# Optimization experiments

Measured on AMD Instinct MI355X. Metric: run time of the kernel, lower is better.

## Reference

```python
import jax, jax.numpy as jnp
import numpy as np

N_SAMPLES = 128
AGENTS = 64
D = 128          # latent_size
EDIM = 2         # edge attr dim
N = N_SAMPLES * AGENTS
EPS = 1e-5


def _build_edges():
    a = np.arange(AGENTS)
    rows = np.repeat(a, AGENTS)
    cols = np.tile(a, AGENTS)
    mask = rows != cols  # fully connected, no self loops
    rows, cols = rows[mask], cols[mask]
    offsets = (np.arange(N_SAMPLES) * AGENTS)[:, None]
    src = (rows[None, :] + offsets).ravel().astype(np.int32)  # edge_index[0]
    dst = (cols[None, :] + offsets).ravel().astype(np.int32)  # edge_index[1]
    return src, dst


def setup_inputs() -> dict:
    key = jax.random.key(0)
    ks = jax.random.split(key, 16)
    src, dst = _build_edges()
    zin = 2 * D + EDIM  # CGConv concat [x_i, x_j, e]
    inp = {
        "gnn_in": jax.random.normal(ks[0], (N, D), jnp.float32),
        "centers": jax.random.normal(ks[1], (N, EDIM), jnp.float32),
        "edge_src": jnp.asarray(src),
        "edge_dst": jnp.asarray(dst),
    }
    for li, base in ((1, 2), (2, 8)):
        inp[f"Wf{li}"] = jax.random.normal(ks[base + 0], (zin, D), jnp.float32) / np.sqrt(zin)
        inp[f"bf{li}"] = jnp.zeros((D,), jnp.float32)
        inp[f"Ws{li}"] = jax.random.normal(ks[base + 1], (zin, D), jnp.float32) / np.sqrt(zin)
        inp[f"bs{li}"] = jnp.zeros((D,), jnp.float32)
        inp[f"gamma{li}"] = jnp.ones((D,), jnp.float32)
        inp[f"beta{li}"] = jnp.zeros((D,), jnp.float32)
    return inp


def _cgconv(x, e, src, dst, Wf, bf, Ws, bs, gamma, beta):
    # message: z = [x_i(target), x_j(source), e]; sigmoid(Wf z) * softplus(Ws z)
    z = jnp.concatenate([x[dst], x[src], e], axis=-1)  # [E, 2D+2]
    m = jax.nn.sigmoid(z @ Wf + bf) * jax.nn.softplus(z @ Ws + bs)
    agg = jax.ops.segment_sum(m, dst, num_segments=N)  # scatter-add at targets
    # batch norm (training-mode batch stats) then residual, as in PyG CGConv
    mu = agg.mean(axis=0)
    var = agg.var(axis=0)
    agg = (agg - mu) * jax.lax.rsqrt(var + EPS) * gamma + beta
    return agg + x


def reference(gnn_in, centers, edge_src, edge_dst,
              Wf1, bf1, Ws1, bs1, gamma1, beta1,
              Wf2, bf2, Ws2, bs2, gamma2, beta2):
    # edge_attr = centers[col] - centers[row]
    e = centers[edge_dst] - centers[edge_src]  # [E, 2]
    x = jax.nn.relu(_cgconv(gnn_in, e, edge_src, edge_dst, Wf1, bf1, Ws1, bs1, gamma1, beta1))
    x = jax.nn.relu(_cgconv(x, e, edge_src, edge_dst, Wf2, bf2, Ws2, bs2, gamma2, beta2))
    return x
```

## Files before the change

kernel.cpp:

```cpp
#include <hip/hip_runtime.h>
#include <hip/hip_bf16.h>

#define NSAMP 128
#define AGENTS 64
#define D 128
#define NN (NSAMP * AGENTS)
#define LOG2E 1.44269504088896340736f
#define LN2   0.69314718055994530942f
#define EPSF  1e-5f

typedef __attribute__((ext_vector_type(8))) short short8;
typedef __attribute__((ext_vector_type(4))) float floatx4;

__device__ __forceinline__ float bf2f(unsigned short u) {
    unsigned v = ((unsigned)u) << 16;
    float f; __builtin_memcpy(&f, &v, 4); return f;
}
__device__ __forceinline__ unsigned short f2bf(float f) {
    unsigned x; __builtin_memcpy(&x, &f, 4);
    return (unsigned short)((x + 0x7FFFu + ((x >> 16) & 1u)) >> 16);
}

__global__ __launch_bounds__(256) void cvt_kernel(
    const float* __restrict__ x0,
    const float* __restrict__ Wf1, const float* __restrict__ Ws1,
    const float* __restrict__ Wf2, const float* __restrict__ Ws2,
    unsigned short* __restrict__ Xb, unsigned short* __restrict__ WT)
{
    int b = blockIdx.x;
    if (b < 512) {
        int off = (b * 256 + threadIdx.x) * 8;
        float4 v0 = *(const float4*)&x0[off];
        float4 v1 = *(const float4*)&x0[off + 4];
        short8 s;
        s[0] = (short)f2bf(v0.x); s[1] = (short)f2bf(v0.y);
        s[2] = (short)f2bf(v0.z); s[3] = (short)f2bf(v0.w);
        s[4] = (short)f2bf(v1.x); s[5] = (short)f2bf(v1.y);
        s[6] = (short)f2bf(v1.z); s[7] = (short)f2bf(v1.w);
        *(short8*)&Xb[off] = s;
    } else {
        int wb = b - 512;
        int rr = wb * 16 + (threadIdx.x >> 4);
        int kk = (threadIdx.x & 15) * 8;
        int layer = rr >> 9, rem = rr & 511, arr = rem >> 7, c = rem & 127;
        const float* M = (arr < 2) ? (layer ? Wf2 : Wf1) : (layer ? Ws2 : Ws1);
        int side = arr & 1;
        short8 s;
        #pragma unroll
        for (int j = 0; j < 8; ++j)
            s[j] = (short)f2bf(M[(size_t)(side * 128 + kk + j) * D + c]);
        *(short8*)&WT[(size_t)(layer * 4 + arr) * 16384 + c * 128 + kk] = s;
    }
}

__global__ __launch_bounds__(256) void prep_mfma(
    const unsigned short* __restrict__ Xb,
    const unsigned short* __restrict__ WT,
    const float* __restrict__ centers,
    const float* __restrict__ Wf, const float* __restrict__ bf_,
    const float* __restrict__ Ws, const float* __restrict__ bs_,
    unsigned short* __restrict__ out)
{
    const int m0   = blockIdx.x * 16;
    const int wv   = threadIdx.x >> 6;
    const int lane = threadIdx.x & 63;
    const int quad = lane >> 4, l16 = lane & 15;

    short8 a[4];
    const unsigned short* xrow = Xb + (size_t)(m0 + l16) * 128 + quad * 8;
    #pragma unroll
    for (int kc = 0; kc < 4; ++kc) a[kc] = *(const short8*)(xrow + kc * 32);

    float ce0[4], ce1[4];
    #pragma unroll
    for (int r = 0; r < 4; ++r) {
        int n = m0 + quad * 4 + r;
        ce0[r] = centers[2 * n]; ce1[r] = centers[2 * n + 1];
    }

    const float sgn   = (wv & 1) ? -1.f : 1.f;
    const float scale = (wv < 2) ? -LOG2E : LOG2E;
    const float* Wsrc = (wv < 2) ? Wf : Ws;
    const float* bias = (wv == 0) ? bf_ : ((wv == 2) ? bs_ : nullptr);
    const unsigned short* Wa = WT + (size_t)wv * 16384;
    unsigned short* ob = out + (size_t)wv * NN * 128;

    for (int nt = 0; nt < 8; ++nt) {
        const int n0 = nt * 16;
        short8 bfr[4];
        const unsigned short* wrow = Wa + (size_t)(n0 + l16) * 128 + quad * 8;
        #pragma unroll
        for (int kc = 0; kc < 4; ++kc) bfr[kc] = *(const short8*)(wrow + kc * 32);

        floatx4 acc = {0.f, 0.f, 0.f, 0.f};
        #pragma unroll
        for (int kc = 0; kc < 4; ++kc)
            acc = __builtin_amdgcn_mfma_f32_16x16x32_bf16(a[kc], bfr[kc], acc, 0, 0, 0);

        const int col = n0 + l16;
        const float cw0 = Wsrc[256 * D + col];
        const float cw1 = Wsrc[257 * D + col];
        const float bv  = bias ? bias[col] : 0.f;
        #pragma unroll
        for (int r = 0; r < 4; ++r) {
            float t = acc[r] + bv + sgn * fmaf(ce0[r], cw0, ce1[r] * cw1);
            ob[(size_t)(m0 + quad * 4 + r) * 128 + col] =
                f2bf(__builtin_amdgcn_exp2f(scale * t));
        }
    }
}

__global__ __launch_bounds__(256) void edge_kernel(
    const unsigned short* __restrict__ EAf, const unsigned short* __restrict__ EBf,
    const unsigned short* __restrict__ EAs, const unsigned short* __restrict__ EBs,
    float* __restrict__ agg,
    float* __restrict__ partials)
{
    const int s = blockIdx.x >> 2;
    const int g = blockIdx.x & 3;
    const int tid = threadIdx.x;
    const int c  = tid & 127;
    const int dh = tid >> 7;
    const int nbase = s * AGENTS;

    __shared__ float Bfs[AGENTS][D];
    __shared__ float Bss[AGENTS][D];

    #pragma unroll
    for (int i = 0; i < 4; ++i) {
        int f8 = i * 256 + tid;
        int idx = f8 * 8;
        int j = idx >> 7, cc = idx & 127;
        short8 vf = *(const short8*)&EBf[(size_t)(nbase + j) * D + cc];
        short8 vs = *(const short8*)&EBs[(size_t)(nbase + j) * D + cc];
        float4 f0, f1, s0, s1v;
        f0.x = bf2f((unsigned short)vf[0]); f0.y = bf2f((unsigned short)vf[1]);
        f0.z = bf2f((unsigned short)vf[2]); f0.w = bf2f((unsigned short)vf[3]);
        f1.x = bf2f((unsigned short)vf[4]); f1.y = bf2f((unsigned short)vf[5]);
        f1.z = bf2f((unsigned short)vf[6]); f1.w = bf2f((unsigned short)vf[7]);
        s0.x = bf2f((unsigned short)vs[0]); s0.y = bf2f((unsigned short)vs[1]);
        s0.z = bf2f((unsigned short)vs[2]); s0.w = bf2f((unsigned short)vs[3]);
        s1v.x = bf2f((unsigned short)vs[4]); s1v.y = bf2f((unsigned short)vs[5]);
        s1v.z = bf2f((unsigned short)vs[6]); s1v.w = bf2f((unsigned short)vs[7]);
        *(float4*)&Bfs[j][cc]     = f0;
        *(float4*)&Bfs[j][cc + 4] = f1;
        *(float4*)&Bss[j][cc]     = s0;
        *(float4*)&Bss[j][cc + 4] = s1v;
    }
    __syncthreads();

    const int d0 = g * 16 + dh * 8;
    float eaf[8], eas[8], acc[8];
    #pragma unroll
    for (int i = 0; i < 8; ++i) {
        int n = nbase + d0 + i;
        eaf[i] = bf2f(EAf[(size_t)n * D + c]);
        eas[i] = bf2f(EAs[(size_t)n * D + c]);
        acc[i] = 0.f;
    }

    for (int j = 0; j < AGENTS; ++j) {
        float ebf = Bfs[j][c];
        float ebs = Bss[j][c];
        #pragma unroll
        for (int i = 0; i < 8; ++i) {
            float sg = __builtin_amdgcn_rcpf(1.f + eaf[i] * ebf);
            float lg = __builtin_amdgcn_logf(1.f + eas[i] * ebs);
            acc[i] += sg * lg;
        }
    }

    float s1 = 0.f, s2 = 0.f;
    #pragma unroll
    for (int i = 0; i < 8; ++i) {
        int j = d0 + i;
        float sg = __builtin_amdgcn_rcpf(1.f + eaf[i] * Bfs[j][c]);
        float lg = __builtin_amdgcn_logf(1.f + eas[i] * Bss[j][c]);
        float a = (acc[i] - sg * lg) * LN2;
        agg[(size_t)(nbase + d0 + i) * D + c] = a;
        s1 += a;
        s2 += a * a;
    }

    __syncthreads();
    if (dh == 1) { Bfs[0][c] = s1; Bss[0][c] = s2; }
    __syncthreads();
    if (dh == 0) {
        s1 += Bfs[0][c];
        s2 += Bss[0][c];
        partials[(size_t)blockIdx.x * 256 + c]       = s1;
        partials[(size_t)blockIdx.x * 256 + 128 + c] = s2;
    }
}

__global__ __launch_bounds__(256) void stats_kernel(
    const float* __restrict__ partials, float* __restrict__ stats)
{
    const int c = blockIdx.x;
    const int t = threadIdx.x;
    float s1 = partials[(size_t)t * 256 + c] + partials[(size_t)(t + 256) * 256 + c];
    float s2 = partials[(size_t)t * 256 + 128 + c] + partials[(size_t)(t + 256) * 256 + 128 + c];
    __shared__ float r1[256], r2[256];
    r1[t] = s1; r2[t] = s2;
    __syncthreads();
    for (int off = 128; off > 0; off >>= 1) {
        if (t < off) { r1[t] += r1[t + off]; r2[t] += r2[t + off]; }
        __syncthreads();
    }
    if (t == 0) {
        float mu = r1[0] * (1.f / NN);
        float var = r2[0] * (1.f / NN) - mu * mu;
        stats[c]     = mu;
        stats[D + c] = rsqrtf(var + EPSF);
    }
}

__global__ __launch_bounds__(256) void bncvt_kernel(
    const float* __restrict__ agg, const float* __restrict__ xin,
    const float* __restrict__ stats,
    const float* __restrict__ gamma, const float* __restrict__ beta,
    float* __restrict__ x1, unsigned short* __restrict__ Xb)
{
    const int t = blockIdx.x * 256 + threadIdx.x;
    const int n = t >> 4;
    const int c = (t & 15) * 8;
    size_t off = (size_t)n * D + c;
    float v[8]; short8 s;
    #pragma unroll
    for (int h = 0; h < 2; ++h) {
        float4 a  = *(const float4*)&agg[off + h * 4];
        float4 xv = *(const float4*)&xin[off + h * 4];
        float4 mu = *(const float4*)&stats[c + h * 4];
        float4 rs = *(const float4*)&stats[D + c + h * 4];
        float4 gm = *(const float4*)&gamma[c + h * 4];
        float4 bt = *(const float4*)&beta[c + h * 4];
        v[h*4+0] = fmaxf(0.f, fmaf((a.x - mu.x) * rs.x, gm.x, bt.x) + xv.x);
        v[h*4+1] = fmaxf(0.f, fmaf((a.y - mu.y) * rs.y, gm.y, bt.y) + xv.y);
        v[h*4+2] = fmaxf(0.f, fmaf((a.z - mu.z) * rs.z, gm.z, bt.z) + xv.z);
        v[h*4+3] = fmaxf(0.f, fmaf((a.w - mu.w) * rs.w, gm.w, bt.w) + xv.w);
    }
    *(float4*)&x1[off]     = *(float4*)&v[0];
    *(float4*)&x1[off + 4] = *(float4*)&v[4];
    #pragma unroll
    for (int e = 0; e < 8; ++e) s[e] = (short)f2bf(v[e]);
    *(short8*)&Xb[off] = s;
}

__global__ __launch_bounds__(256) void bn_kernel(
    const float* __restrict__ agg, const float* __restrict__ xin,
    const float* __restrict__ stats,
    const float* __restrict__ gamma, const float* __restrict__ beta,
    float* __restrict__ outp)
{
    const int t = blockIdx.x * 256 + threadIdx.x;
    const int n = t >> 5;
    const int c = (t & 31) * 4;
    float4 a  = *(const float4*)&agg[(size_t)n * D + c];
    float4 xv = *(const float4*)&xin[(size_t)n * D + c];
    float4 mu = *(const float4*)&stats[c];
    float4 rs = *(const float4*)&stats[D + c];
    float4 gm = *(const float4*)&gamma[c];
    float4 bt = *(const float4*)&beta[c];
    float4 o;
    o.x = fmaxf(0.f, fmaf((a.x - mu.x) * rs.x, gm.x, bt.x) + xv.x);
    o.y = fmaxf(0.f, fmaf((a.y - mu.y) * rs.y, gm.y, bt.y) + xv.y);
    o.z = fmaxf(0.f, fmaf((a.z - mu.z) * rs.z, gm.z, bt.z) + xv.z);
    o.w = fmaxf(0.f, fmaf((a.w - mu.w) * rs.w, gm.w, bt.w) + xv.w);
    *(float4*)&outp[(size_t)n * D + c] = o;
}

extern "C" void kernel_launch(void* const* d_in, const int* in_sizes, int n_in,
                              void* d_out, int out_size, void* d_ws, size_t ws_size,
                              hipStream_t stream) {
    const float* x0      = (const float*)d_in[0];
    const float* centers = (const float*)d_in[1];
    const float* Wf[2] = { (const float*)d_in[4],  (const float*)d_in[10] };
    const float* bf[2] = { (const float*)d_in[5],  (const float*)d_in[11] };
    const float* Ws[2] = { (const float*)d_in[6],  (const float*)d_in[12] };
    const float* bs[2] = { (const float*)d_in[7],  (const float*)d_in[13] };
    const float* gm[2] = { (const float*)d_in[8],  (const float*)d_in[14] };
    const float* bt[2] = { (const float*)d_in[9],  (const float*)d_in[15] };

    const size_t ND = (size_t)NN * D;
    unsigned short* ws_u = (unsigned short*)d_ws;
    unsigned short* Xb = ws_u;
    unsigned short* WT = ws_u + ND;
    unsigned short* AB = WT + 2 * 65536;
    float* fbase    = (float*)(AB + 4 * ND);
    float* agg      = fbase;
    float* x1       = fbase + ND;
    float* partials = fbase + 2 * ND;
    float* stats    = partials + 512 * 256;

    float* outp = (float*)d_out;

    cvt_kernel<<<dim3(576), dim3(256), 0, stream>>>(
        x0, Wf[0], Ws[0], Wf[1], Ws[1], Xb, WT);

    prep_mfma<<<dim3(512), dim3(256), 0, stream>>>(
        Xb, WT, centers, Wf[0], bf[0], Ws[0], bs[0], AB);
    edge_kernel<<<dim3(512), dim3(256), 0, stream>>>(
        AB, AB + ND, AB + 2 * ND, AB + 3 * ND, agg, partials);
    stats_kernel<<<dim3(128), dim3(256), 0, stream>>>(partials, stats);
    bncvt_kernel<<<dim3(512), dim3(256), 0, stream>>>(
        agg, x0, stats, gm[0], bt[0], x1, Xb);

    prep_mfma<<<dim3(512), dim3(256), 0, stream>>>(
        Xb, WT + 65536, centers, Wf[1], bf[1], Ws[1], bs[1], AB);
    edge_kernel<<<dim3(512), dim3(256), 0, stream>>>(
        AB, AB + ND, AB + 2 * ND, AB + 3 * ND, agg, partials);
    stats_kernel<<<dim3(128), dim3(256), 0, stream>>>(partials, stats);
    bn_kernel<<<dim3(1024), dim3(256), 0, stream>>>(
        agg, x1, stats, gm[1], bt[1], outp);
}
```

Measured before the change: 165.2 us.

## Fuse projection GEMM into edge kernel and replace stats pass with atomics

Merges the MFMA projection kernel into the edge kernel. Each block now computes its sample's source-side exponentials directly into shared memory as packed bf16 pairs, and computes the target-side values for its own 16 rows, so the bf16 intermediate buffers never go through global memory. The separate stats reduction kernel is replaced by per-block atomicAdd into a zeroed accumulator, with mean and rsqrt folded into the BN kernels. This saves two launches per layer and the intermediate traffic. In exchange, each of the 4 blocks per sample recomputes the 64-row source GEMM, and float atomics make the sums order-nondeterministic.

```diff
diff --git a/kernel.cpp b/kernel.cpp
--- a/kernel.cpp
+++ b/kernel.cpp
@@ -12,8 +12,7 @@
 typedef __attribute__((ext_vector_type(8))) short short8;
 typedef __attribute__((ext_vector_type(4))) float floatx4;
 
-__device__ __forceinline__ float bf2f(unsigned short u) {
-    unsigned v = ((unsigned)u) << 16;
+__device__ __forceinline__ float u2f(unsigned v) {
     float f; __builtin_memcpy(&f, &v, 4); return f;
 }
 __device__ __forceinline__ unsigned short f2bf(float f) {
@@ -25,7 +24,8 @@
     const float* __restrict__ x0,
     const float* __restrict__ Wf1, const float* __restrict__ Ws1,
     const float* __restrict__ Wf2, const float* __restrict__ Ws2,
-    unsigned short* __restrict__ Xb, unsigned short* __restrict__ WT)
+    unsigned short* __restrict__ Xb, unsigned short* __restrict__ WT,
+    float* __restrict__ sacc)
 {
     int b = blockIdx.x;
     if (b < 512) {
@@ -38,7 +38,7 @@
         s[4] = (short)f2bf(v1.x); s[5] = (short)f2bf(v1.y);
         s[6] = (short)f2bf(v1.z); s[7] = (short)f2bf(v1.w);
         *(short8*)&Xb[off] = s;
-    } else {
+    } else if (b < 576) {
         int wb = b - 512;
         int rr = wb * 16 + (threadIdx.x >> 4);
         int kk = (threadIdx.x & 15) * 8;
@@ -50,174 +50,147 @@
         for (int j = 0; j < 8; ++j)
             s[j] = (short)f2bf(M[(size_t)(side * 128 + kk + j) * D + c]);
         *(short8*)&WT[(size_t)(layer * 4 + arr) * 16384 + c * 128 + kk] = s;
-    }
-}
-
-__global__ __launch_bounds__(256) void prep_mfma(
+    } else {
+        sacc[threadIdx.x]       = 0.f;
+        sacc[256 + threadIdx.x] = 0.f;
+    }
+}
+
+__global__ __launch_bounds__(256) void prep_edge(
     const unsigned short* __restrict__ Xb,
     const unsigned short* __restrict__ WT,
     const float* __restrict__ centers,
     const float* __restrict__ Wf, const float* __restrict__ bf_,
     const float* __restrict__ Ws, const float* __restrict__ bs_,
-    unsigned short* __restrict__ out)
-{
-    const int m0   = blockIdx.x * 16;
-    const int wv   = threadIdx.x >> 6;
-    const int lane = threadIdx.x & 63;
+    float* __restrict__ agg,
+    float* __restrict__ sacc)
+{
+    const int s = blockIdx.x >> 2, g = blockIdx.x & 3;
+    const int nbase = s * AGENTS;
+    const int tid = threadIdx.x, wv = tid >> 6, lane = tid & 63;
     const int quad = lane >> 4, l16 = lane & 15;
 
-    short8 a[4];
-    const unsigned short* xrow = Xb + (size_t)(m0 + l16) * 128 + quad * 8;
-    #pragma unroll
-    for (int kc = 0; kc < 4; ++kc) a[kc] = *(const short8*)(xrow + kc * 32);
-
-    float ce0[4], ce1[4];
-    #pragma unroll
-    for (int r = 0; r < 4; ++r) {
-        int n = m0 + quad * 4 + r;
-        ce0[r] = centers[2 * n]; ce1[r] = centers[2 * n + 1];
-    }
-
-    const float sgn   = (wv & 1) ? -1.f : 1.f;
-    const float scale = (wv < 2) ? -LOG2E : LOG2E;
-    const float* Wsrc = (wv < 2) ? Wf : Ws;
-    const float* bias = (wv == 0) ? bf_ : ((wv == 2) ? bs_ : nullptr);
-    const unsigned short* Wa = WT + (size_t)wv * 16384;
-    unsigned short* ob = out + (size_t)wv * NN * 128;
-
-    for (int nt = 0; nt < 8; ++nt) {
-        const int n0 = nt * 16;
-        short8 bfr[4];
-        const unsigned short* wrow = Wa + (size_t)(n0 + l16) * 128 + quad * 8;
-        #pragma unroll
-        for (int kc = 0; kc < 4; ++kc) bfr[kc] = *(const short8*)(wrow + kc * 32);
-
-        floatx4 acc = {0.f, 0.f, 0.f, 0.f};
-        #pragma unroll
-        for (int kc = 0; kc < 4; ++kc)
-            acc = __builtin_amdgcn_mfma_f32_16x16x32_bf16(a[kc], bfr[kc], acc, 0, 0, 0);
-
-        const int col = n0 + l16;
-        const float cw0 = Wsrc[256 * D + col];
-        const float cw1 = Wsrc[257 * D + col];
-        const float bv  = bias ? bias[col] : 0.f;
+    __shared__ float        EAls[2][16][132];
+    __shared__ unsigned int EBpk[64][132];
+
+    short8 wBf[2][4], wBs[2][4];
+    float cwf0[2], cwf1[2], cws0[2], cws1[2], bfv[2], bsv[2];
+    #pragma unroll
+    for (int p = 0; p < 2; ++p) {
+        const int col = wv * 32 + p * 16 + l16;
+        const unsigned short* w1 = WT + (size_t)1 * 16384 + (size_t)col * 128 + quad * 8;
+        const unsigned short* w3 = WT + (size_t)3 * 16384 + (size_t)col * 128 + quad * 8;
+        #pragma unroll
+        for (int kc = 0; kc < 4; ++kc) {
+            wBf[p][kc] = *(const short8*)(w1 + kc * 32);
+            wBs[p][kc] = *(const short8*)(w3 + kc * 32);
+        }
+        cwf0[p] = Wf[256 * D + col]; cwf1[p] = Wf[257 * D + col];
+        cws0[p] = Ws[256 * D + col]; cws1[p] = Ws[257 * D + col];
+        bfv[p] = bf_[col]; bsv[p] = bs_[col];
+    }
+
+    for (int m = 0; m < 4; ++m) {
+        short8 a[4];
+        const unsigned short* xr = Xb + (size_t)(nbase + m * 16 + l16) * 128 + quad * 8;
+        #pragma unroll
+        for (int kc = 0; kc < 4; ++kc) a[kc] = *(const short8*)(xr + kc * 32);
+        float ce0[4], ce1[4];
         #pragma unroll
         for (int r = 0; r < 4; ++r) {
-            float t = acc[r] + bv + sgn * fmaf(ce0[r], cw0, ce1[r] * cw1);
-            ob[(size_t)(m0 + quad * 4 + r) * 128 + col] =
-                f2bf(__builtin_amdgcn_exp2f(scale * t));
-        }
-    }
-}
-
-__global__ __launch_bounds__(256) void edge_kernel(
-    const unsigned short* __restrict__ EAf, const unsigned short* __restrict__ EBf,
-    const unsigned short* __restrict__ EAs, const unsigned short* __restrict__ EBs,
-    float* __restrict__ agg,
-    float* __restrict__ partials)
-{
-    const int s = blockIdx.x >> 2;
-    const int g = blockIdx.x & 3;
-    const int tid = threadIdx.x;
-    const int c  = tid & 127;
-    const int dh = tid >> 7;
-    const int nbase = s * AGENTS;
-
-    __shared__ float Bfs[AGENTS][D];
-    __shared__ float Bss[AGENTS][D];
-
-    #pragma unroll
-    for (int i = 0; i < 4; ++i) {
-        int f8 = i * 256 + tid;
-        int idx = f8 * 8;
-        int j = idx >> 7, cc = idx & 127;
-        short8 vf = *(const short8*)&EBf[(size_t)(nbase + j) * D + cc];
-        short8 vs = *(const short8*)&EBs[(size_t)(nbase + j) * D + cc];
-        float4 f0, f1, s0, s1v;
-        f0.x = bf2f((unsigned short)vf[0]); f0.y = bf2f((unsigned short)vf[1]);
-        f0.z = bf2f((unsigned short)vf[2]); f0.w = bf2f((unsigned short)vf[3]);
-        f1.x = bf2f((unsigned short)vf[4]); f1.y = bf2f((unsigned short)vf[5]);
-        f1.z = bf2f((unsigned short)vf[6]); f1.w = bf2f((unsigned short)vf[7]);
-        s0.x = bf2f((unsigned short)vs[0]); s0.y = bf2f((unsigned short)vs[1]);
-        s0.z = bf2f((unsigned short)vs[2]); s0.w = bf2f((unsigned short)vs[3]);
-        s1v.x = bf2f((unsigned short)vs[4]); s1v.y = bf2f((unsigned short)vs[5]);
-        s1v.z = bf2f((unsigned short)vs[6]); s1v.w = bf2f((unsigned short)vs[7]);
-        *(float4*)&Bfs[j][cc]     = f0;
-        *(float4*)&Bfs[j][cc + 4] = f1;
-        *(float4*)&Bss[j][cc]     = s0;
-        *(float4*)&Bss[j][cc + 4] = s1v;
+            int n = nbase + m * 16 + quad * 4 + r;
+            ce0[r] = centers[2 * n]; ce1[r] = centers[2 * n + 1];
+        }
+        #pragma unroll
+        for (int p = 0; p < 2; ++p) {
+            floatx4 aF = {0.f,0.f,0.f,0.f}, aS = {0.f,0.f,0.f,0.f};
+            #pragma unroll
+            for (int kc = 0; kc < 4; ++kc) {
+                aF = __builtin_amdgcn_mfma_f32_16x16x32_bf16(a[kc], wBf[p][kc], aF, 0,0,0);
+                aS = __builtin_amdgcn_mfma_f32_16x16x32_bf16(a[kc], wBs[p][kc], aS, 0,0,0);
+            }
+            const int col = wv * 32 + p * 16 + l16;
+            #pragma unroll
+            for (int r = 0; r < 4; ++r) {
+                float ctf = fmaf(ce0[r], cwf0[p], ce1[r] * cwf1[p]);
+                float cts = fmaf(ce0[r], cws0[p], ce1[r] * cws1[p]);
+                unsigned uf = (unsigned)f2bf(__builtin_amdgcn_exp2f(-LOG2E * (aF[r] - ctf)));
+                unsigned us = (unsigned)f2bf(__builtin_amdgcn_exp2f( LOG2E * (aS[r] - cts)));
+                EBpk[m * 16 + quad * 4 + r][col] = uf | (us << 16);
+            }
+        }
+        if (m == g) {
+            #pragma unroll
+            for (int p = 0; p < 2; ++p) {
+                const int col = wv * 32 + p * 16 + l16;
+                const unsigned short* w0 = WT + (size_t)col * 128 + quad * 8;
+                const unsigned short* w2 = WT + (size_t)2 * 16384 + (size_t)col * 128 + quad * 8;
+                floatx4 aF = {0.f,0.f,0.f,0.f}, aS = {0.f,0.f,0.f,0.f};
+                #pragma unroll
+                for (int kc = 0; kc < 4; ++kc) {
+                    short8 f0 = *(const short8*)(w0 + kc * 32);
+                    short8 f2 = *(const short8*)(w2 + kc * 32);
+                    aF = __builtin_amdgcn_mfma_f32_16x16x32_bf16(a[kc], f0, aF, 0,0,0);
+                    aS = __builtin_amdgcn_mfma_f32_16x16x32_bf16(a[kc], f2, aS, 0,0,0);
+                }
+                #pragma unroll
+                for (int r = 0; r < 4; ++r) {
+                    float ctf = fmaf(ce0[r], cwf0[p], ce1[r] * cwf1[p]);
+                    float cts = fmaf(ce0[r], cws0[p], ce1[r] * cws1[p]);
+                    EAls[0][quad * 4 + r][col] =
+                        __builtin_amdgcn_exp2f(-LOG2E * (aF[r] + ctf + bfv[p]));
+                    EAls[1][quad * 4 + r][col] =
+                        __builtin_amdgcn_exp2f( LOG2E * (aS[r] + cts + bsv[p]));
+                }
+            }
+        }
     }
     __syncthreads();
 
-    const int d0 = g * 16 + dh * 8;
+    const int c = tid & 127, dh = tid >> 7;
     float eaf[8], eas[8], acc[8];
     #pragma unroll
     for (int i = 0; i < 8; ++i) {
-        int n = nbase + d0 + i;
-        eaf[i] = bf2f(EAf[(size_t)n * D + c]);
-        eas[i] = bf2f(EAs[(size_t)n * D + c]);
+        eaf[i] = EAls[0][dh * 8 + i][c];
+        eas[i] = EAls[1][dh * 8 + i][c];
         acc[i] = 0.f;
     }
-
-    for (int j = 0; j < AGENTS; ++j) {
-        float ebf = Bfs[j][c];
-        float ebs = Bss[j][c];
+    for (int j = 0; j < 64; ++j) {
+        unsigned pk = EBpk[j][c];
+        float ebf = u2f(pk << 16);
+        float ebs = u2f(pk & 0xFFFF0000u);
         #pragma unroll
         for (int i = 0; i < 8; ++i) {
-            float sg = __builtin_amdgcn_rcpf(1.f + eaf[i] * ebf);
-            float lg = __builtin_amdgcn_logf(1.f + eas[i] * ebs);
-            acc[i] += sg * lg;
-        }
-    }
-
+            float sg = __builtin_amdgcn_rcpf(fmaf(eaf[i], ebf, 1.f));
+            float lg = __builtin_amdgcn_logf(fmaf(eas[i], ebs, 1.f));
+            acc[i] = fmaf(sg, lg, acc[i]);
+        }
+    }
     float s1 = 0.f, s2 = 0.f;
     #pragma unroll
     for (int i = 0; i < 8; ++i) {
-        int j = d0 + i;
-        float sg = __builtin_amdgcn_rcpf(1.f + eaf[i] * Bfs[j][c]);
-        float lg = __builtin_amdgcn_logf(1.f + eas[i] * Bss[j][c]);
+        int dl = g * 16 + dh * 8 + i;
+        unsigned pk = EBpk[dl][c];
+        float ebf = u2f(pk << 16);
+        float ebs = u2f(pk & 0xFFFF0000u);
+        float sg = __builtin_amdgcn_rcpf(fmaf(eaf[i], ebf, 1.f));
+        float lg = __builtin_amdgcn_logf(fmaf(eas[i], ebs, 1.f));
         float a = (acc[i] - sg * lg) * LN2;
-        agg[(size_t)(nbase + d0 + i) * D + c] = a;
-        s1 += a;
-        s2 += a * a;
-    }
-
+        agg[(size_t)(nbase + dl) * D + c] = a;
+        s1 += a; s2 += a * a;
+    }
     __syncthreads();
-    if (dh == 1) { Bfs[0][c] = s1; Bss[0][c] = s2; }
+    if (dh == 1) { EAls[0][0][c] = s1; EAls[0][1][c] = s2; }
     __syncthreads();
     if (dh == 0) {
-        s1 += Bfs[0][c];
-        s2 += Bss[0][c];
-        partials[(size_t)blockIdx.x * 256 + c]       = s1;
-        partials[(size_t)blockIdx.x * 256 + 128 + c] = s2;
-    }
-}
-
-__global__ __launch_bounds__(256) void stats_kernel(
-    const float* __restrict__ partials, float* __restrict__ stats)
-{
-    const int c = blockIdx.x;
-    const int t = threadIdx.x;
-    float s1 = partials[(size_t)t * 256 + c] + partials[(size_t)(t + 256) * 256 + c];
-    float s2 = partials[(size_t)t * 256 + 128 + c] + partials[(size_t)(t + 256) * 256 + 128 + c];
-    __shared__ float r1[256], r2[256];
-    r1[t] = s1; r2[t] = s2;
-    __syncthreads();
-    for (int off = 128; off > 0; off >>= 1) {
-        if (t < off) { r1[t] += r1[t + off]; r2[t] += r2[t + off]; }
-        __syncthreads();
-    }
-    if (t == 0) {
-        float mu = r1[0] * (1.f / NN);
-        float var = r2[0] * (1.f / NN) - mu * mu;
-        stats[c]     = mu;
-        stats[D + c] = rsqrtf(var + EPSF);
+        atomicAdd(&sacc[c],       s1 + EAls[0][0][c]);
+        atomicAdd(&sacc[128 + c], s2 + EAls[0][1][c]);
     }
 }
 
 __global__ __launch_bounds__(256) void bncvt_kernel(
     const float* __restrict__ agg, const float* __restrict__ xin,
-    const float* __restrict__ stats,
+    const float* __restrict__ sacc,
     const float* __restrict__ gamma, const float* __restrict__ beta,
     float* __restrict__ x1, unsigned short* __restrict__ Xb)
 {
@@ -225,48 +198,65 @@
     const int n = t >> 4;
     const int c = (t & 15) * 8;
     size_t off = (size_t)n * D + c;
-    float v[8]; short8 s;
+    const float inv = 1.f / NN;
+    float v[8]; short8 sv;
     #pragma unroll
     for (int h = 0; h < 2; ++h) {
         float4 a  = *(const float4*)&agg[off + h * 4];
         float4 xv = *(const float4*)&xin[off + h * 4];
-        float4 mu = *(const float4*)&stats[c + h * 4];
-        float4 rs = *(const float4*)&stats[D + c + h * 4];
+        float4 s1 = *(const float4*)&sacc[c + h * 4];
+        float4 s2 = *(const float4*)&sacc[128 + c + h * 4];
         float4 gm = *(const float4*)&gamma[c + h * 4];
         float4 bt = *(const float4*)&beta[c + h * 4];
-        v[h*4+0] = fmaxf(0.f, fmaf((a.x - mu.x) * rs.x, gm.x, bt.x) + xv.x);
-        v[h*4+1] = fmaxf(0.f, fmaf((a.y - mu.y) * rs.y, gm.y, bt.y) + xv.y);
-        v[h*4+2] = fmaxf(0.f, fmaf((a.z - mu.z) * rs.z, gm.z, bt.z) + xv.z);
-        v[h*4+3] = fmaxf(0.f, fmaf((a.w - mu.w) * rs.w, gm.w, bt.w) + xv.w);
+        float mu, var, rs;
+        mu = s1.x * inv; var = s2.x * inv - mu * mu; rs = rsqrtf(var + EPSF);
+        v[h*4+0] = fmaxf(0.f, fmaf((a.x - mu) * rs, gm.x, bt.x) + xv.x);
+        mu = s1.y * inv; var = s2.y * inv - mu * mu; rs = rsqrtf(var + EPSF);
+        v[h*4+1] = fmaxf(0.f, fmaf((a.y - mu) * rs, gm.y, bt.y) + xv.y);
+        mu = s1.z * inv; var = s2.z * inv - mu * mu; rs = rsqrtf(var + EPSF);
+        v[h*4+2] = fmaxf(0.f, fmaf((a.z - mu) * rs, gm.z, bt.z) + xv.z);
+        mu = s1.w * inv; var = s2.w * inv - mu * mu; rs = rsqrtf(var + EPSF);
+        v[h*4+3] = fmaxf(0.f, fmaf((a.w - mu) * rs, gm.w, bt.w) + xv.w);
     }
     *(float4*)&x1[off]     = *(float4*)&v[0];
     *(float4*)&x1[off + 4] = *(float4*)&v[4];
     #pragma unroll
-    for (int e = 0; e < 8; ++e) s[e] = (short)f2bf(v[e]);
-    *(short8*)&Xb[off] = s;
+    for (int e = 0; e < 8; ++e) sv[e] = (short)f2bf(v[e]);
+    *(short8*)&Xb[off] = sv;
 }
 
 __global__ __launch_bounds__(256) void bn_kernel(
     const float* __restrict__ agg, const float* __restrict__ xin,
-    const float* __restrict__ stats,
+    const float* __restrict__ sacc,
     const float* __restrict__ gamma, const float* __restrict__ beta,
     float* __restrict__ outp)
 {
     const int t = blockIdx.x * 256 + threadIdx.x;
-    const int n = t >> 5;
-    const int c = (t & 31) * 4;
-    float4 a  = *(const float4*)&agg[(size_t)n * D + c];
-    float4 xv = *(const float4*)&xin[(size_t)n * D + c];
-    float4 mu = *(const float4*)&stats[c];
-    float4 rs = *(const float4*)&stats[D + c];
-    float4 gm = *(const float4*)&gamma[c];
-    float4 bt = *(const float4*)&beta[c];
-    float4 o;
-    o.x = fmaxf(0.f, fmaf((a.x - mu.x) * rs.x, gm.x, bt.x) + xv.x);
-    o.y = fmaxf(0.f, fmaf((a.y - mu.y) * rs.y, gm.y, bt.y) + xv.y);
-    o.z = fmaxf(0.f, fmaf((a.z - mu.z) * rs.z, gm.z, bt.z) + xv.z);
-    o.w = fmaxf(0.f, fmaf((a.w - mu.w) * rs.w, gm.w, bt.w) + xv.w);
-    *(float4*)&outp[(size_t)n * D + c] = o;
+    const int n = t >> 4;
+    const int c = (t & 15) * 8;
+    size_t off = (size_t)n * D + c;
+    const float inv = 1.f / NN;
+    float v[8];
+    #pragma unroll
+    for (int h = 0; h < 2; ++h) {
+        float4 a  = *(const float4*)&agg[off + h * 4];
+        float4 xv = *(const float4*)&xin[off + h * 4];
+        float4 s1 = *(const float4*)&sacc[c + h * 4];
+        float4 s2 = *(const float4*)&sacc[128 + c + h * 4];
+        float4 gm = *(const float4*)&gamma[c + h * 4];
+        float4 bt = *(const float4*)&beta[c + h * 4];
+        float mu, var, rs;
+        mu = s1.x * inv; var = s2.x * inv - mu * mu; rs = rsqrtf(var + EPSF);
+        v[h*4+0] = fmaxf(0.f, fmaf((a.x - mu) * rs, gm.x, bt.x) + xv.x);
+        mu = s1.y * inv; var = s2.y * inv - mu * mu; rs = rsqrtf(var + EPSF);
+        v[h*4+1] = fmaxf(0.f, fmaf((a.y - mu) * rs, gm.y, bt.y) + xv.y);
+        mu = s1.z * inv; var = s2.z * inv - mu * mu; rs = rsqrtf(var + EPSF);
+        v[h*4+2] = fmaxf(0.f, fmaf((a.z - mu) * rs, gm.z, bt.z) + xv.z);
+        mu = s1.w * inv; var = s2.w * inv - mu * mu; rs = rsqrtf(var + EPSF);
+        v[h*4+3] = fmaxf(0.f, fmaf((a.w - mu) * rs, gm.w, bt.w) + xv.w);
+    }
+    *(float4*)&outp[off]     = *(float4*)&v[0];
+    *(float4*)&outp[off + 4] = *(float4*)&v[4];
 }
 
 extern "C" void kernel_launch(void* const* d_in, const int* in_sizes, int n_in,
@@ -285,31 +275,23 @@
     unsigned short* ws_u = (unsigned short*)d_ws;
     unsigned short* Xb = ws_u;
     unsigned short* WT = ws_u + ND;
-    unsigned short* AB = WT + 2 * 65536;
-    float* fbase    = (float*)(AB + 4 * ND);
-    float* agg      = fbase;
-    float* x1       = fbase + ND;
-    float* partials = fbase + 2 * ND;
-    float* stats    = partials + 512 * 256;
+    float* fbase = (float*)(WT + 2 * 65536);
+    float* agg   = fbase;
+    float* x1    = fbase + ND;
+    float* sacc  = fbase + 2 * ND;
 
     float* outp = (float*)d_out;
 
-    cvt_kernel<<<dim3(576), dim3(256), 0, stream>>>(
-        x0, Wf[0], Ws[0], Wf[1], Ws[1], Xb, WT);
-
-    prep_mfma<<<dim3(512), dim3(256), 0, stream>>>(
-        Xb, WT, centers, Wf[0], bf[0], Ws[0], bs[0], AB);
-    edge_kernel<<<dim3(512), dim3(256), 0, stream>>>(
-        AB, AB + ND, AB + 2 * ND, AB + 3 * ND, agg, partials);
-    stats_kernel<<<dim3(128), dim3(256), 0, stream>>>(partials, stats);
+    cvt_kernel<<<dim3(577), dim3(256), 0, stream>>>(
+        x0, Wf[0], Ws[0], Wf[1], Ws[1], Xb, WT, sacc);
+
+    prep_edge<<<dim3(512), dim3(256), 0, stream>>>(
+        Xb, WT, centers, Wf[0], bf[0], Ws[0], bs[0], agg, sacc);
     bncvt_kernel<<<dim3(512), dim3(256), 0, stream>>>(
-        agg, x0, stats, gm[0], bt[0], x1, Xb);
-
-    prep_mfma<<<dim3(512), dim3(256), 0, stream>>>(
-        Xb, WT + 65536, centers, Wf[1], bf[1], Ws[1], bs[1], AB);
-    edge_kernel<<<dim3(512), dim3(256), 0, stream>>>(
-        AB, AB + ND, AB + 2 * ND, AB + 3 * ND, agg, partials);
-    stats_kernel<<<dim3(128), dim3(256), 0, stream>>>(partials, stats);
-    bn_kernel<<<dim3(1024), dim3(256), 0, stream>>>(
-        agg, x1, stats, gm[1], bt[1], outp);
-}
+        agg, x0, sacc, gm[0], bt[0], x1, Xb);
+
+    prep_edge<<<dim3(512), dim3(256), 0, stream>>>(
+        Xb, WT + 65536, centers, Wf[1], bf[1], Ws[1], bs[1], agg, sacc + 256);
+    bn_kernel<<<dim3(512), dim3(256), 0, stream>>>(
+        agg, x1, sacc + 256, gm[1], bt[1], outp);
+}
```

Result: no change. 163.1 us (-1.3%).
